# Kernel tuning notes

Hardware: AMD Instinct MI355X
Metric: run time of the kernel (lower is better)

The kernel has to match this reference:

```python
import jax, jax.numpy as jnp
import numpy as np

D = 1024
D_HEAD = 64
N_PC = 1024
N_JOINTS = 128
L = N_PC + N_JOINTS  # 1152, == max_seq_len so cache read == fresh k/v at start_pos=0
N_HEADS = D // D_HEAD


def _block_mask():
    # True = attend. pc tokens attend pc tokens (full); joint tokens attend all pc
    # tokens plus causal among joints; pc tokens never attend joint tokens.
    i = jnp.arange(L)[:, None]
    j = jnp.arange(L)[None, :]
    return (j < N_PC) | ((i >= N_PC) & (j >= N_PC) & (j <= i))


def setup_inputs() -> dict:
    key = jax.random.key(0)
    kx, kqkv, kfc = jax.random.split(key, 3)
    s = 1.0 / np.sqrt(D)
    x = jax.random.normal(kx, (1, L, D), dtype=jnp.float32)
    w_qkv = jax.random.normal(kqkv, (3 * D, D), dtype=jnp.float32) * s  # torch Linear weight [out,in]
    w_fc = jax.random.normal(kfc, (D, D), dtype=jnp.float32) * s
    return {"x": x, "w_qkv": w_qkv, "w_fc": w_fc}


def reference(x, w_qkv, w_fc):
    b, l, _ = x.shape
    qkv = jnp.einsum('bld,ed->ble', x, w_qkv)  # [b, l, 3d]
    q, k, v = jnp.split(qkv, 3, axis=-1)

    def heads(t):  # [b, l, d] -> [b, nh, l, dh]
        return t.reshape(b, l, N_HEADS, D_HEAD).transpose(0, 2, 1, 3)

    q, k, v = heads(q), heads(k), heads(v)
    # KV-cache write + read at start_pos=0 with seq_len==max_seq_len is identity.
    scale = 1.0 / np.sqrt(D_HEAD)
    scores = jnp.einsum('bhqd,bhkd->bhqk', q, k) * scale
    mask = _block_mask()
    scores = jnp.where(mask[None, None, :, :], scores, jnp.finfo(scores.dtype).min)
    attn = jax.nn.softmax(scores, axis=-1)
    out = jnp.einsum('bhqk,bhkd->bhqd', attn, v)  # [b, nh, l, dh]
    out = out.transpose(0, 2, 1, 3).reshape(b, l, D)
    return jnp.einsum('bld,ed->ble', out, w_fc)
```

## Files before the change

kernel.cpp:

```cpp
#include <hip/hip_runtime.h>
#include <hip/hip_bf16.h>


typedef short bf16x8 __attribute__((ext_vector_type(8)));
typedef float f32x4 __attribute__((ext_vector_type(4)));
typedef float f32x16 __attribute__((ext_vector_type(16)));

#define L_SEQ   1152
#define NPC     1024
#define DMODEL  1024
#define TD      3072
#define NHEADS  16
#define DHEAD   64
#define NT32    36

__device__ __forceinline__ void gld_lds16(const void* g, void* l) {
  __builtin_amdgcn_global_load_lds((const __attribute__((address_space(1))) void*)g,
                                   (__attribute__((address_space(3))) void*)l,
                                   16, 0, 0);
}

template <int N>
__device__ __forceinline__ void s_wait_vmcnt() {
  if constexpr (N == 0)       asm volatile("s_waitcnt vmcnt(0)" ::: "memory");
  else if constexpr (N == 2)  asm volatile("s_waitcnt vmcnt(2)" ::: "memory");
  else if constexpr (N == 4)  asm volatile("s_waitcnt vmcnt(4)" ::: "memory");
  else if constexpr (N == 6)  asm volatile("s_waitcnt vmcnt(6)" ::: "memory");
  else if constexpr (N == 8)  asm volatile("s_waitcnt vmcnt(8)" ::: "memory");
  else if constexpr (N == 12) asm volatile("s_waitcnt vmcnt(12)" ::: "memory");
  else if constexpr (N == 16) asm volatile("s_waitcnt vmcnt(16)" ::: "memory");
  else static_assert(N == 0, "add vmcnt case");
}

__global__ void cvt_all(const float* __restrict__ x, const float* __restrict__ wq,
                        const float* __restrict__ wf,
                        __hip_bfloat16* __restrict__ xb,
                        __hip_bfloat16* __restrict__ wqb,
                        __hip_bfloat16* __restrict__ wfb) {
  const int NX = 1152 * 1024 / 4, NQ = 3072 * 1024 / 4;
  int i = blockIdx.x * blockDim.x + threadIdx.x;
  const float* s; __hip_bfloat16* d; int j;
  if (i < NX) { s = x; d = xb; j = i; }
  else if (i < NX + NQ) { s = wq; d = wqb; j = i - NX; }
  else { s = wf; d = wfb; j = i - NX - NQ; }
  float4 v = ((const float4*)s)[j];
  __align__(8) __hip_bfloat16 o[4];
  o[0] = __float2bfloat16(v.x);
  o[1] = __float2bfloat16(v.y);
  o[2] = __float2bfloat16(v.z);
  o[3] = __float2bfloat16(v.w);
  *(uint2*)&d[(size_t)j * 4] = *(const uint2*)o;
}

template <int BM, int BN, int MODE, typename OT>
__global__ __launch_bounds__(256) void gemm_bt(
    const __hip_bfloat16* __restrict__ A,
    const __hip_bfloat16* __restrict__ B,
    OT* __restrict__ C, __hip_bfloat16* __restrict__ kT,
    __hip_bfloat16* __restrict__ vT,
    int M, int N, int K, int MT) {
  constexpr int WMT = BM / 2, WNT = BN / 2;
  constexpr int MI = WMT / 16, NI = WNT / 16;
  constexpr int ACH = BM * 8, BCH = BN * 8;
  constexpr int S = (ACH + BCH) / 256;
  __shared__ __align__(16) __hip_bfloat16 As[3][BM * 64];
  __shared__ __align__(16) __hip_bfloat16 Bs[3][BN * 64];

  const int tid = threadIdx.x, lane = tid & 63, w = tid >> 6;
  const int wm = w >> 1, wn = w & 1, l15 = lane & 15, lg = lane >> 4;
  const int chunk = (int)gridDim.x >> 3;
  const int wgid = ((int)blockIdx.x & 7) * chunk + ((int)blockIdx.x >> 3);
  const int m0 = (wgid % MT) * BM, n0 = (wgid / MT) * BN;

  f32x4 acc[MI][NI] = {};

  auto stage = [&](int b, int kt) {
    const __hip_bfloat16* Ag = A + (size_t)m0 * K + kt;
    const __hip_bfloat16* Bg = B + (size_t)n0 * K + kt;
#pragma unroll
    for (int c = tid; c < ACH; c += 256) {
      int r = c >> 3, gc = (c & 7) ^ (r & 7);
      gld_lds16(Ag + (size_t)r * K + gc * 8, &As[b][c * 8]);
    }
#pragma unroll
    for (int c = tid; c < BCH; c += 256) {
      int r = c >> 3, gc = (c & 7) ^ (r & 7);
      gld_lds16(Bg + (size_t)r * K + gc * 8, &Bs[b][c * 8]);
    }
  };

  const int NK = K >> 6;
  stage(0, 0);
  stage(1, 64);
  stage(2, 128);

  int buf = 0;
  for (int t = 0; t < NK; ++t) {
    if (t < NK - 2)       s_wait_vmcnt<2 * S>();
    else if (t == NK - 2) s_wait_vmcnt<S>();
    else                  s_wait_vmcnt<0>();
    __builtin_amdgcn_s_barrier();
    __builtin_amdgcn_sched_barrier(0);

#pragma unroll
    for (int kk = 0; kk < 2; ++kk) {
      bf16x8 af[MI], bfr[NI];
#pragma unroll
      for (int i = 0; i < MI; ++i) {
        int r = wm * WMT + i * 16 + l15;
        af[i] = *(const bf16x8*)&As[buf][(r * 8 + (((kk << 2) + lg) ^ (r & 7))) * 8];
      }
#pragma unroll
      for (int i = 0; i < NI; ++i) {
        int r = wn * WNT + i * 16 + l15;
        bfr[i] = *(const bf16x8*)&Bs[buf][(r * 8 + (((kk << 2) + lg) ^ (r & 7))) * 8];
      }
#pragma unroll
      for (int mi = 0; mi < MI; ++mi)
#pragma unroll
        for (int ni = 0; ni < NI; ++ni)
          acc[mi][ni] = __builtin_amdgcn_mfma_f32_16x16x32_bf16(
              af[mi], bfr[ni], acc[mi][ni], 0, 0, 0);
    }

    __builtin_amdgcn_sched_barrier(0);
    __builtin_amdgcn_s_barrier();
    __builtin_amdgcn_sched_barrier(0);
    if (t + 3 < NK) stage(buf, (t + 3) * 64);
    buf = (buf + 1 == 3) ? 0 : buf + 1;
  }

  if constexpr (MODE == 0) {
#pragma unroll
    for (int mi = 0; mi < MI; ++mi)
#pragma unroll
      for (int ni = 0; ni < NI; ++ni) {
        int rb = m0 + wm * WMT + mi * 16 + lg * 4;
        int cb = n0 + wn * WNT + ni * 16 + l15;
#pragma unroll
        for (int r = 0; r < 4; ++r)
          C[(size_t)(rb + r) * N + cb] = acc[mi][ni][r];
      }
  } else if (n0 < 2 * DMODEL) {
    const bool isQ = (n0 < DMODEL);
    const float scl = isQ ? 0.18033688f : 1.0f;
    __hip_bfloat16* dst = isQ ? (__hip_bfloat16*)C : kT;
    const int nb = isQ ? n0 : (n0 - DMODEL);
    constexpr int TS2 = BN + 8;
    __hip_bfloat16* T = &As[0][0];
    __syncthreads();
#pragma unroll
    for (int mi = 0; mi < MI; ++mi)
#pragma unroll
      for (int ni = 0; ni < NI; ++ni) {
        int ml = wm * WMT + mi * 16 + lg * 4;
        int nl = wn * WNT + ni * 16 + l15;
#pragma unroll
        for (int r = 0; r < 4; ++r)
          T[(ml + r) * TS2 + nl] = __float2bfloat16(acc[mi][ni][r] * scl);
      }
    __syncthreads();
#pragma unroll
    for (int c = tid; c < (BM * BN) / 8; c += 256) {
      int ml = c >> 4, dc = c & 15;
      bf16x8 v = *(const bf16x8*)&T[ml * TS2 + dc * 8];
      int dfull = nb + dc * 8;
      int hh = dfull >> 6, dh = dfull & 63;
      int g = m0 + ml;
      size_t off = ((size_t)(hh * NT32 + (g >> 5))) * 2048 +
                   (size_t)((dh >> 4) * 64 + ((dh >> 3) & 1) * 32 + (g & 31)) * 8;
      *(bf16x8*)&dst[off] = v;
    }
  } else {
    constexpr int TS = BM + 8;
    __hip_bfloat16* T = &As[0][0];
    __syncthreads();
#pragma unroll
    for (int mi = 0; mi < MI; ++mi)
#pragma unroll
      for (int ni = 0; ni < NI; ++ni) {
        int e = wn * WNT + ni * 16 + l15;
        int l = wm * WMT + mi * 16 + lg * 4;
        __align__(8) __hip_bfloat16 o4[4];
#pragma unroll
        for (int r = 0; r < 4; ++r) o4[r] = __float2bfloat16(acc[mi][ni][r]);
        *(uint2*)&T[e * TS + l] = *(const uint2*)o4;
      }
    __syncthreads();
#pragma unroll
    for (int c = tid; c < (BN * BM) / 8; c += 256) {
      int dl = c >> 3, kvc = (c & 7) * 8;
      bf16x8 v = *(const bf16x8*)&T[dl * TS + kvc];
      int dfull = n0 - 2 * DMODEL + dl;
      int hh = dfull >> 6, dh = dfull & 63;
      int kvg = m0 + kvc;
      size_t off = ((size_t)(hh * NT32 + (kvg >> 5))) * 2048 +
                   (size_t)((((kvg >> 4) & 1) * 2 + (dh >> 5)) * 64 +
                            ((kvg >> 3) & 1) * 32 + (dh & 31)) * 8;
      *(bf16x8*)&vT[off] = v;
    }
  }
}

__global__ __launch_bounds__(128) void attn32(
    const __hip_bfloat16* __restrict__ qT,
    const __hip_bfloat16* __restrict__ kT,
    const __hip_bfloat16* __restrict__ vT,
    __hip_bfloat16* __restrict__ attnb) {
  const int wgid = ((int)blockIdx.x & 7) * 72 + ((int)blockIdx.x >> 3);
  const int h = wgid / NT32, qt = wgid % NT32;
  const int q0 = qt * 32;
  const int tid = threadIdx.x, lane = tid & 63, w = tid >> 6;
  const int l31 = lane & 31, hi = lane >> 5;

  __shared__ __align__(16) float Osh[2][32][68];
  __shared__ float Lsh[2][32];

  const __hip_bfloat16* qtp = qT + ((size_t)h * NT32 + qt) * 2048;
  bf16x8 qf0 = *(const bf16x8*)(qtp + (0 * 64 + lane) * 8);
  bf16x8 qf1 = *(const bf16x8*)(qtp + (1 * 64 + lane) * 8);
  bf16x8 qf2 = *(const bf16x8*)(qtp + (2 * 64 + lane) * 8);
  bf16x8 qf3 = *(const bf16x8*)(qtp + (3 * 64 + lane) * 8);

  const int q = q0 + l31;
  const int lim = (q < NPC) ? NPC : (q + 1);
  const int nst = (q0 < NPC) ? 32 : ((q0 + 32) >> 5);
  const int tbeg = (w * nst) >> 1, tend = ((w + 1) * nst) >> 1;

  const __hip_bfloat16* ktp = kT + (size_t)h * NT32 * 2048;
  const __hip_bfloat16* vtp = vT + (size_t)h * NT32 * 2048;

  float lsum = 0.f;
  f32x16 oA = {}, oB = {};
  bf16x8 kA[4], vA[4], kB[4], vB[4];
  float p[16];
  bf16x8 pa0, pa1;

  auto LDk = [&](bf16x8 (&kf)[4], int t) {
    const __hip_bfloat16* kp = ktp + (size_t)t * 2048;
#pragma unroll
    for (int c = 0; c < 4; ++c) kf[c] = *(const bf16x8*)(kp + (c * 64 + lane) * 8);
  };
  auto LDv = [&](bf16x8 (&vf)[4], int t) {
    const __hip_bfloat16* vp = vtp + (size_t)t * 2048;
#pragma unroll
    for (int c = 0; c < 4; ++c) vf[c] = *(const bf16x8*)(vp + (c * 64 + lane) * 8);
  };

  auto QK = [&](bf16x8 (&kf)[4]) -> f32x16 {
    f32x16 S0 = {}, S1 = {};
    __builtin_amdgcn_s_setprio(1);
    S0 = __builtin_amdgcn_mfma_f32_32x32x16_bf16(kf[0], qf0, S0, 0, 0, 0);
    S1 = __builtin_amdgcn_mfma_f32_32x32x16_bf16(kf[2], qf2, S1, 0, 0, 0);
    S0 = __builtin_amdgcn_mfma_f32_32x32x16_bf16(kf[1], qf1, S0, 0, 0, 0);
    S1 = __builtin_amdgcn_mfma_f32_32x32x16_bf16(kf[3], qf3, S1, 0, 0, 0);
    __builtin_amdgcn_s_setprio(0);
    return S0 + S1;
  };

  auto FIN = [&](const f32x16& S, int t) {
#pragma unroll
    for (int r = 0; r < 16; ++r) p[r] = __builtin_amdgcn_exp2f(S[r]);
    const int kv0 = t << 5;
    if (kv0 >= NPC) {
#pragma unroll
      for (int r = 0; r < 16; ++r) {
        int kv = kv0 + (r & 3) + 8 * (r >> 2) + 4 * hi;
        if (kv >= lim) p[r] = 0.f;
      }
    }
#pragma unroll
    for (int r = 0; r < 16; ++r) lsum += p[r];
  };

  auto PACK = [&]() {
    unsigned W[8];
#pragma unroll
    for (int g = 0; g < 2; ++g) {
      unsigned x0, x1, y0, y1;
      asm("v_cvt_pk_bf16_f32 %0, %1, %2" : "=v"(x0) : "v"(p[g*8+0]), "v"(p[g*8+1]));
      asm("v_cvt_pk_bf16_f32 %0, %1, %2" : "=v"(x1) : "v"(p[g*8+4]), "v"(p[g*8+5]));
      asm("v_cvt_pk_bf16_f32 %0, %1, %2" : "=v"(y0) : "v"(p[g*8+2]), "v"(p[g*8+3]));
      asm("v_cvt_pk_bf16_f32 %0, %1, %2" : "=v"(y1) : "v"(p[g*8+6]), "v"(p[g*8+7]));
      asm("v_permlane32_swap_b32 %0, %1" : "+v"(x0), "+v"(x1));
      asm("v_permlane32_swap_b32 %0, %1" : "+v"(y0), "+v"(y1));
      W[g*4+0] = x0; W[g*4+1] = y0; W[g*4+2] = x1; W[g*4+3] = y1;
    }
    __builtin_memcpy(&pa0, &W[0], 16);
    __builtin_memcpy(&pa1, &W[4], 16);
  };

  auto PV = [&](bf16x8 (&vf)[4]) {
    __builtin_amdgcn_s_setprio(1);
    oA = __builtin_amdgcn_mfma_f32_32x32x16_bf16(pa0, vf[0], oA, 0, 0, 0);
    oB = __builtin_amdgcn_mfma_f32_32x32x16_bf16(pa0, vf[1], oB, 0, 0, 0);
    oA = __builtin_amdgcn_mfma_f32_32x32x16_bf16(pa1, vf[2], oA, 0, 0, 0);
    oB = __builtin_amdgcn_mfma_f32_32x32x16_bf16(pa1, vf[3], oB, 0, 0, 0);
    __builtin_amdgcn_s_setprio(0);
  };

  LDk(kA, tbeg); LDv(vA, tbeg);
  LDk(kB, tbeg + 1); LDv(vB, tbeg + 1);
  f32x16 S = QK(kA);
  int st = tbeg;
  for (; st + 2 <= tend; st += 2) {
    f32x16 S2 = QK(kB);
    if (st + 2 < tend) LDk(kA, st + 2);
    FIN(S, st); PACK(); PV(vA);
    if (st + 2 < tend) LDv(vA, st + 2);
    if (st + 2 < tend) S = QK(kA);
    if (st + 3 < tend) LDk(kB, st + 3);
    FIN(S2, st + 1); PACK(); PV(vB);
    if (st + 3 < tend) LDv(vB, st + 3);
  }
  if (st < tend) { FIN(S, st); PACK(); PV(vA); }

  lsum += __shfl_xor(lsum, 32);

#pragma unroll
  for (int r = 0; r < 16; ++r) {
    int qr = (r & 3) + 8 * (r >> 2) + 4 * hi;
    Osh[w][qr][l31] = oA[r];
    Osh[w][qr][32 + l31] = oB[r];
  }
  if (lane < 32) Lsh[w][l31] = lsum;
  __syncthreads();

  const int qq = tid >> 2, d16 = (tid & 3) * 16;
  float inv = 1.0f / (Lsh[0][qq] + Lsh[1][qq]);
#pragma unroll
  for (int g = 0; g < 2; ++g) {
    __align__(16) __hip_bfloat16 o8[8];
#pragma unroll
    for (int j = 0; j < 8; ++j) {
      float o = Osh[0][qq][d16 + g * 8 + j] + Osh[1][qq][d16 + g * 8 + j];
      o8[j] = __float2bfloat16(o * inv);
    }
    *(int4*)&attnb[(size_t)(q0 + qq) * DMODEL + h * DHEAD + d16 + g * 8] =
        *(const int4*)o8;
  }
}

extern "C" void kernel_launch(void* const* d_in, const int* in_sizes, int n_in,
                              void* d_out, int out_size, void* d_ws, size_t ws_size,
                              hipStream_t stream) {
  const float* x     = (const float*)d_in[0];
  const float* w_qkv = (const float*)d_in[1];
  const float* w_fc  = (const float*)d_in[2];
  float* out = (float*)d_out;

  char* ws = (char*)d_ws;
  __hip_bfloat16* xb    = (__hip_bfloat16*)(ws + 0);
  __hip_bfloat16* wqkvb = (__hip_bfloat16*)(ws + 2359296);
  __hip_bfloat16* wfcb  = (__hip_bfloat16*)(ws + 8650752);
  __hip_bfloat16* qTb   = (__hip_bfloat16*)(ws + 10747904);
  __hip_bfloat16* kTb   = (__hip_bfloat16*)(ws + 13107200);
  __hip_bfloat16* vTb   = (__hip_bfloat16*)(ws + 15466496);
  __hip_bfloat16* attnb = (__hip_bfloat16*)(ws + 17825792);

  cvt_all<<<5248, 256, 0, stream>>>(x, w_qkv, w_fc, xb, wqkvb, wfcb);

  gemm_bt<64, 128, 1, __hip_bfloat16><<<432, 256, 0, stream>>>(
      xb, wqkvb, qTb, kTb, vTb, L_SEQ, TD, DMODEL, 18);

  attn32<<<576, 128, 0, stream>>>(qTb, kTb, vTb, attnb);

  gemm_bt<64, 64, 0, float><<<288, 256, 0, stream>>>(
      attnb, wfcb, out, nullptr, nullptr, L_SEQ, DMODEL, DMODEL, 18);
}
```

Before: 56.71 us.

## Process 64 query rows per attention block with four waves splitting KV

The attention kernel now gives each workgroup 64 query rows as two 32-row halves, running 4 waves that split the KV tiles. Each loaded K/V tile is reused for both query halves, which halves K/V global traffic per query. The two-tile register double-buffering is replaced by a single-buffer loop that prefetches only the next tile, so less load latency may be hidden. LDS use grows to about 70KB for the four-way partial-sum reduction, and the grid shrinks to 288 larger blocks.

```diff
diff --git a/kernel.cpp b/kernel.cpp
--- a/kernel.cpp
+++ b/kernel.cpp
@@ -202,63 +202,66 @@
   }
 }
 
-__global__ __launch_bounds__(128) void attn32(
+__global__ __launch_bounds__(256) void attn64(
     const __hip_bfloat16* __restrict__ qT,
     const __hip_bfloat16* __restrict__ kT,
     const __hip_bfloat16* __restrict__ vT,
     __hip_bfloat16* __restrict__ attnb) {
-  const int wgid = ((int)blockIdx.x & 7) * 72 + ((int)blockIdx.x >> 3);
-  const int h = wgid / NT32, qt = wgid % NT32;
-  const int q0 = qt * 32;
+  const int wgid = ((int)blockIdx.x & 7) * 36 + ((int)blockIdx.x >> 3);
+  const int h = wgid / 18, qt = wgid % 18;
+  const int q0 = qt * 64;
   const int tid = threadIdx.x, lane = tid & 63, w = tid >> 6;
   const int l31 = lane & 31, hi = lane >> 5;
 
-  __shared__ __align__(16) float Osh[2][32][68];
-  __shared__ float Lsh[2][32];
-
-  const __hip_bfloat16* qtp = qT + ((size_t)h * NT32 + qt) * 2048;
-  bf16x8 qf0 = *(const bf16x8*)(qtp + (0 * 64 + lane) * 8);
-  bf16x8 qf1 = *(const bf16x8*)(qtp + (1 * 64 + lane) * 8);
-  bf16x8 qf2 = *(const bf16x8*)(qtp + (2 * 64 + lane) * 8);
-  bf16x8 qf3 = *(const bf16x8*)(qtp + (3 * 64 + lane) * 8);
-
-  const int q = q0 + l31;
-  const int lim = (q < NPC) ? NPC : (q + 1);
-  const int nst = (q0 < NPC) ? 32 : ((q0 + 32) >> 5);
-  const int tbeg = (w * nst) >> 1, tend = ((w + 1) * nst) >> 1;
+  __shared__ __align__(16) float Osh[4][64][68];
+  __shared__ float Lsh[4][64];
+
+  const __hip_bfloat16* qtpLo = qT + ((size_t)h * NT32 + qt * 2) * 2048;
+  const __hip_bfloat16* qtpHi = qtpLo + 2048;
+  bf16x8 qLo[4], qHi[4];
+#pragma unroll
+  for (int c = 0; c < 4; ++c) {
+    qLo[c] = *(const bf16x8*)(qtpLo + (c * 64 + lane) * 8);
+    qHi[c] = *(const bf16x8*)(qtpHi + (c * 64 + lane) * 8);
+  }
+
+  const int limLo = (q0 + l31 < NPC) ? NPC : (q0 + l31 + 1);
+  const int limHi = (q0 + 32 + l31 < NPC) ? NPC : (q0 + 32 + l31 + 1);
+  const int nst = (q0 + 64 <= NPC) ? 32 : ((q0 + 64) >> 5);
+  const int tbeg = (w * nst) >> 2, tend = ((w + 1) * nst) >> 2;
 
   const __hip_bfloat16* ktp = kT + (size_t)h * NT32 * 2048;
   const __hip_bfloat16* vtp = vT + (size_t)h * NT32 * 2048;
 
-  float lsum = 0.f;
-  f32x16 oA = {}, oB = {};
-  bf16x8 kA[4], vA[4], kB[4], vB[4];
+  float lsumLo = 0.f, lsumHi = 0.f;
+  f32x16 oLoA = {}, oLoB = {}, oHiA = {}, oHiB = {};
+  bf16x8 kA[4], vA[4];
   float p[16];
   bf16x8 pa0, pa1;
 
-  auto LDk = [&](bf16x8 (&kf)[4], int t) {
+  auto LDk = [&](int t) {
     const __hip_bfloat16* kp = ktp + (size_t)t * 2048;
 #pragma unroll
-    for (int c = 0; c < 4; ++c) kf[c] = *(const bf16x8*)(kp + (c * 64 + lane) * 8);
-  };
-  auto LDv = [&](bf16x8 (&vf)[4], int t) {
+    for (int c = 0; c < 4; ++c) kA[c] = *(const bf16x8*)(kp + (c * 64 + lane) * 8);
+  };
+  auto LDv = [&](int t) {
     const __hip_bfloat16* vp = vtp + (size_t)t * 2048;
 #pragma unroll
-    for (int c = 0; c < 4; ++c) vf[c] = *(const bf16x8*)(vp + (c * 64 + lane) * 8);
-  };
-
-  auto QK = [&](bf16x8 (&kf)[4]) -> f32x16 {
+    for (int c = 0; c < 4; ++c) vA[c] = *(const bf16x8*)(vp + (c * 64 + lane) * 8);
+  };
+
+  auto QK = [&](bf16x8 (&qf)[4]) -> f32x16 {
     f32x16 S0 = {}, S1 = {};
     __builtin_amdgcn_s_setprio(1);
-    S0 = __builtin_amdgcn_mfma_f32_32x32x16_bf16(kf[0], qf0, S0, 0, 0, 0);
-    S1 = __builtin_amdgcn_mfma_f32_32x32x16_bf16(kf[2], qf2, S1, 0, 0, 0);
-    S0 = __builtin_amdgcn_mfma_f32_32x32x16_bf16(kf[1], qf1, S0, 0, 0, 0);
-    S1 = __builtin_amdgcn_mfma_f32_32x32x16_bf16(kf[3], qf3, S1, 0, 0, 0);
+    S0 = __builtin_amdgcn_mfma_f32_32x32x16_bf16(kA[0], qf[0], S0, 0, 0, 0);
+    S1 = __builtin_amdgcn_mfma_f32_32x32x16_bf16(kA[2], qf[2], S1, 0, 0, 0);
+    S0 = __builtin_amdgcn_mfma_f32_32x32x16_bf16(kA[1], qf[1], S0, 0, 0, 0);
+    S1 = __builtin_amdgcn_mfma_f32_32x32x16_bf16(kA[3], qf[3], S1, 0, 0, 0);
     __builtin_amdgcn_s_setprio(0);
     return S0 + S1;
   };
 
-  auto FIN = [&](const f32x16& S, int t) {
+  auto FIN = [&](const f32x16& S, int t, int lim, float& lsum) {
 #pragma unroll
     for (int r = 0; r < 16; ++r) p[r] = __builtin_amdgcn_exp2f(S[r]);
     const int kv0 = t << 5;
@@ -290,50 +293,51 @@
     __builtin_memcpy(&pa1, &W[4], 16);
   };
 
-  auto PV = [&](bf16x8 (&vf)[4]) {
+  auto PV = [&](f32x16& oA, f32x16& oB) {
     __builtin_amdgcn_s_setprio(1);
-    oA = __builtin_amdgcn_mfma_f32_32x32x16_bf16(pa0, vf[0], oA, 0, 0, 0);
-    oB = __builtin_amdgcn_mfma_f32_32x32x16_bf16(pa0, vf[1], oB, 0, 0, 0);
-    oA = __builtin_amdgcn_mfma_f32_32x32x16_bf16(pa1, vf[2], oA, 0, 0, 0);
-    oB = __builtin_amdgcn_mfma_f32_32x32x16_bf16(pa1, vf[3], oB, 0, 0, 0);
+    oA = __builtin_amdgcn_mfma_f32_32x32x16_bf16(pa0, vA[0], oA, 0, 0, 0);
+    oB = __builtin_amdgcn_mfma_f32_32x32x16_bf16(pa0, vA[1], oB, 0, 0, 0);
+    oA = __builtin_amdgcn_mfma_f32_32x32x16_bf16(pa1, vA[2], oA, 0, 0, 0);
+    oB = __builtin_amdgcn_mfma_f32_32x32x16_bf16(pa1, vA[3], oB, 0, 0, 0);
     __builtin_amdgcn_s_setprio(0);
   };
 
-  LDk(kA, tbeg); LDv(vA, tbeg);
-  LDk(kB, tbeg + 1); LDv(vB, tbeg + 1);
-  f32x16 S = QK(kA);
-  int st = tbeg;
-  for (; st + 2 <= tend; st += 2) {
-    f32x16 S2 = QK(kB);
-    if (st + 2 < tend) LDk(kA, st + 2);
-    FIN(S, st); PACK(); PV(vA);
-    if (st + 2 < tend) LDv(vA, st + 2);
-    if (st + 2 < tend) S = QK(kA);
-    if (st + 3 < tend) LDk(kB, st + 3);
-    FIN(S2, st + 1); PACK(); PV(vB);
-    if (st + 3 < tend) LDv(vB, st + 3);
-  }
-  if (st < tend) { FIN(S, st); PACK(); PV(vA); }
-
-  lsum += __shfl_xor(lsum, 32);
+  LDk(tbeg); LDv(tbeg);
+  for (int st = tbeg; st < tend; ++st) {
+    f32x16 Sl = QK(qLo);
+    f32x16 Sh = QK(qHi);
+    if (st + 1 < tend) LDk(st + 1);
+    FIN(Sl, st, limLo, lsumLo); PACK(); PV(oLoA, oLoB);
+    FIN(Sh, st, limHi, lsumHi); PACK(); PV(oHiA, oHiB);
+    if (st + 1 < tend) LDv(st + 1);
+  }
+
+  lsumLo += __shfl_xor(lsumLo, 32);
+  lsumHi += __shfl_xor(lsumHi, 32);
 
 #pragma unroll
   for (int r = 0; r < 16; ++r) {
     int qr = (r & 3) + 8 * (r >> 2) + 4 * hi;
-    Osh[w][qr][l31] = oA[r];
-    Osh[w][qr][32 + l31] = oB[r];
-  }
-  if (lane < 32) Lsh[w][l31] = lsum;
+    Osh[w][qr][l31]      = oLoA[r];
+    Osh[w][qr][32 + l31] = oLoB[r];
+    Osh[w][32 + qr][l31]      = oHiA[r];
+    Osh[w][32 + qr][32 + l31] = oHiB[r];
+  }
+  if (lane < 32) {
+    Lsh[w][l31] = lsumLo;
+    Lsh[w][32 + l31] = lsumHi;
+  }
   __syncthreads();
 
   const int qq = tid >> 2, d16 = (tid & 3) * 16;
-  float inv = 1.0f / (Lsh[0][qq] + Lsh[1][qq]);
+  float inv = 1.0f / (Lsh[0][qq] + Lsh[1][qq] + Lsh[2][qq] + Lsh[3][qq]);
 #pragma unroll
   for (int g = 0; g < 2; ++g) {
     __align__(16) __hip_bfloat16 o8[8];
 #pragma unroll
     for (int j = 0; j < 8; ++j) {
-      float o = Osh[0][qq][d16 + g * 8 + j] + Osh[1][qq][d16 + g * 8 + j];
+      float o = Osh[0][qq][d16 + g * 8 + j] + Osh[1][qq][d16 + g * 8 + j] +
+                Osh[2][qq][d16 + g * 8 + j] + Osh[3][qq][d16 + g * 8 + j];
       o8[j] = __float2bfloat16(o * inv);
     }
     *(int4*)&attnb[(size_t)(q0 + qq) * DMODEL + h * DHEAD + d16 + g * 8] =
@@ -363,7 +367,7 @@
   gemm_bt<64, 128, 1, __hip_bfloat16><<<432, 256, 0, stream>>>(
       xb, wqkvb, qTb, kTb, vTb, L_SEQ, TD, DMODEL, 18);
 
-  attn32<<<576, 128, 0, stream>>>(qTb, kTb, vTb, attnb);
+  attn64<<<288, 256, 0, stream>>>(qTb, kTb, vTb, attnb);
 
   gemm_bt<64, 64, 0, float><<<288, 256, 0, stream>>>(
       attnb, wfcb, out, nullptr, nullptr, L_SEQ, DMODEL, DMODEL, 18);
```

After: 59.70 us. +5.3%, slower.
